# Kernel tuning notes

Hardware: AMD Instinct MI355X
Metric: run time of the kernel (lower is better)

## Reference

```python
import jax, jax.numpy as jnp
import numpy as np

EMBED_DIM = 512
N_HEADS = 8
HEAD_DIM = EMBED_DIM // N_HEADS
SEQ = 4096
BATCH = 2


def setup_inputs() -> dict:
    key = jax.random.key(0)
    k1, k2, k3 = jax.random.split(key, 3)
    x = jax.random.normal(k1, (SEQ, BATCH, EMBED_DIM), dtype=jnp.float32)
    # xavier_uniform for [3E, E]: limit = sqrt(6/(3E+E))
    lim_in = float(np.sqrt(6.0 / (3 * EMBED_DIM + EMBED_DIM)))
    in_proj_weight = jax.random.uniform(k2, (3 * EMBED_DIM, EMBED_DIM), minval=-lim_in, maxval=lim_in, dtype=jnp.float32)
    in_proj_bias = jnp.zeros((3 * EMBED_DIM,), jnp.float32)
    lim_out = float(np.sqrt(1.0 / EMBED_DIM))  # torch Linear default init range
    out_weight = jax.random.uniform(k3, (EMBED_DIM, EMBED_DIM), minval=-lim_out, maxval=lim_out, dtype=jnp.float32)
    out_bias = jnp.zeros((EMBED_DIM,), jnp.float32)
    return {"x": x, "in_proj_weight": in_proj_weight, "in_proj_bias": in_proj_bias,
            "out_weight": out_weight, "out_bias": out_bias}


def reference(x, in_proj_weight, in_proj_bias, out_weight, out_bias):
    # x: [S, B, E] (seq-first, as in the torch module)
    S, B, E = x.shape
    H, D = N_HEADS, HEAD_DIM
    scaling = 1.0 / (D ** 0.5)
    qkv = x @ in_proj_weight.T + in_proj_bias            # [S, B, 3E]
    q, k, v = jnp.split(qkv, 3, axis=-1)                 # each [S, B, E]
    # reshape to [B*H, S, D]
    def to_bh(t):
        return t.reshape(S, B * H, D).transpose(1, 0, 2)
    q = to_bh(q * scaling)
    k = to_bh(k)
    v = to_bh(v)
    scores = jnp.einsum('bqd,bkd->bqk', q, k)            # [B*H, S, S]
    attn = jax.nn.softmax(scores, axis=-1)
    out = jnp.einsum('bqk,bkd->bqd', attn, v)            # [B*H, S, D]
    out = out.transpose(1, 0, 2).reshape(S, B, E)        # [S, B, E]
    return out @ out_weight.T + out_bias
```

## Files before the change

### kernel.cpp

```cpp
#include <hip/hip_runtime.h>

typedef unsigned short u16;
typedef unsigned int   u32;
typedef short bf16x8 __attribute__((ext_vector_type(8)));
typedef float f32x2  __attribute__((ext_vector_type(2)));
typedef float f32x4  __attribute__((ext_vector_type(4)));
typedef float f32x16 __attribute__((ext_vector_type(16)));
typedef u32   u32x4  __attribute__((ext_vector_type(4)));

#define QK_SCALE 0.18033688011112042f

__device__ __forceinline__ u16 f2bf(float f) {
  u32 u = __builtin_bit_cast(u32, f);
  u = (u + 0x7FFFu + ((u >> 16) & 1u)) >> 16;
  return (u16)u;
}

__device__ __forceinline__ u32 cvtpk(float lo, float hi) {
  u32 r;
  asm("v_cvt_pk_bf16_f32 %0, %1, %2" : "=v"(r) : "v"(lo), "v"(hi));
  return r;
}

__device__ __forceinline__ void gload16(void* lds, const void* g) {
  __builtin_amdgcn_global_load_lds(
      (const __attribute__((address_space(1))) u32*)g,
      (__attribute__((address_space(3))) u32*)lds, 16, 0, 0);
}

__device__ __forceinline__ bf16x8 ld8(const void* p) {
  return *(const bf16x8*)p;
}

__global__ __launch_bounds__(256) void cvt_kernel(
    const float* __restrict__ x, const float* __restrict__ w1,
    const float* __restrict__ w2,
    u16* __restrict__ xb, u16* __restrict__ wb, u16* __restrict__ ob) {
  int i = blockIdx.x * 256 + threadIdx.x;
  const float* src; u16* dst; int off;
  if (i < 1048576)            { src = x;  dst = xb; off = i; }
  else if (i < 1048576+196608){ src = w1; dst = wb; off = i - 1048576; }
  else                        { src = w2; dst = ob; off = i - 1245184; }
  float4 v = ((const float4*)src)[off];
  ushort4 o;
  o.x = f2bf(v.x); o.y = f2bf(v.y); o.z = f2bf(v.z); o.w = f2bf(v.w);
  ((ushort4*)dst)[off] = o;
}

template<int MODE>
__global__ __launch_bounds__(256, 2) void gemm_bt(
    const u16* __restrict__ A, const u16* __restrict__ Bm,
    const float* __restrict__ bias,
    u16* __restrict__ q_out, u16* __restrict__ k_out, u16* __restrict__ v_out,
    float* __restrict__ f_out, int M, int N, int K) {
  __shared__ __attribute__((aligned(16))) u16 As[128 * 64];
  __shared__ __attribute__((aligned(16))) u16 Bs[128 * 64];
  const int tid = threadIdx.x, lane = tid & 63, w = tid >> 6;
  const int wm = w >> 1, wn = w & 1;
  const int lo = lane & 15, hi = lane >> 4;
  const int m0 = blockIdx.x * 128, n0 = blockIdx.y * 128;
  f32x4 acc[4][4] = {};
  const int srow = lane >> 3;
  const int skc  = (lane & 7) ^ srow;
  const int nk = K >> 6;
  for (int kt = 0; kt < nk; ++kt) {
    __syncthreads();
    const int k0 = kt * 64;
#pragma unroll
    for (int c = 0; c < 4; ++c) {
      const int ch = w * 4 + c;
      const int row = ch * 8 + srow;
      gload16((char*)As + ch * 1024, A  + (size_t)(m0 + row) * K + k0 + skc * 8);
      gload16((char*)Bs + ch * 1024, Bm + (size_t)(n0 + row) * K + k0 + skc * 8);
    }
    __syncthreads();
#pragma unroll
    for (int kk = 0; kk < 2; ++kk) {
      bf16x8 af[4], bfr[4];
#pragma unroll
      for (int mi = 0; mi < 4; ++mi) {
        const int row = wm * 64 + mi * 16 + lo;
        const int kc = kk * 4 + hi;
        af[mi] = ld8((const char*)As + row * 128 + ((kc ^ (row & 7)) << 4));
      }
#pragma unroll
      for (int ni = 0; ni < 4; ++ni) {
        const int row = wn * 64 + ni * 16 + lo;
        const int kc = kk * 4 + hi;
        bfr[ni] = ld8((const char*)Bs + row * 128 + ((kc ^ (row & 7)) << 4));
      }
#pragma unroll
      for (int mi = 0; mi < 4; ++mi)
#pragma unroll
        for (int ni = 0; ni < 4; ++ni)
          acc[mi][ni] = __builtin_amdgcn_mfma_f32_16x16x32_bf16(
              af[mi], bfr[ni], acc[mi][ni], 0, 0, 0);
    }
  }
#pragma unroll
  for (int mi = 0; mi < 4; ++mi)
#pragma unroll
    for (int ni = 0; ni < 4; ++ni) {
      const int gn = n0 + wn * 64 + ni * 16 + lo;
      const float bv = bias[gn];
#pragma unroll
      for (int r = 0; r < 4; ++r) {
        const int gm = m0 + wm * 64 + mi * 16 + hi * 4 + r;
        float val = acc[mi][ni][r] + bv;
        if (MODE == 0) {
          const int s = gm >> 1, b = gm & 1;
          const int sec = gn >> 9, e = gn & 511;
          const int h = e >> 6, d = e & 63;
          const size_t o = (((size_t)(b * 8 + h) * 4096 + s) << 6) + d;
          if (sec == 0)      q_out[o] = f2bf(val * QK_SCALE);
          else if (sec == 1) k_out[o] = f2bf(val);
          else               v_out[o] = f2bf(val);
        } else {
          f_out[(size_t)gm * N + gn] = val;
        }
      }
    }
}

__global__ __launch_bounds__(256) void transpose_v(
    const u16* __restrict__ v, u16* __restrict__ vt) {
  __shared__ __attribute__((aligned(16))) u16 T[64 * 72];
  const int bh = blockIdx.y, s0 = blockIdx.x * 64;
  const int t = threadIdx.x;
#pragma unroll
  for (int i = 0; i < 2; ++i) {
    const int idx = t + i * 256;
    const int row = idx >> 3, c = idx & 7;
    uint4 d = *(const uint4*)(v + ((size_t)bh * 4096 + s0 + row) * 64 + c * 8);
    *(uint4*)(&T[row * 72 + c * 8]) = d;
  }
  __syncthreads();
#pragma unroll
  for (int i = 0; i < 2; ++i) {
    const int idx = t + i * 256;
    const int dcol = idx >> 3, sc = idx & 7;
    u16 tmp[8];
#pragma unroll
    for (int j = 0; j < 8; ++j) tmp[j] = T[(sc * 8 + j) * 72 + dcol];
    *(uint4*)(vt + ((size_t)bh * 64 + dcol) * 4096 + s0 + sc * 8) = *(const uint4*)tmp;
  }
}

__global__ __launch_bounds__(256, 4) void fa_kernel(
    const u16* __restrict__ q, const u16* __restrict__ k,
    const u16* __restrict__ vt, u16* __restrict__ attn) {
  __shared__ __attribute__((aligned(16))) char S_lds[2][2][8192];
  const int tid = threadIdx.x, lane = tid & 63, w = tid >> 6;
  const int lo = lane & 31, hi5 = lane >> 5;
  const int wq = w & 1;
  const int kvh = w >> 1;
  const int wg = blockIdx.x;
  const int xcd = wg & 7, idx = wg >> 3;
  const int bh = xcd * 2 + (idx >> 6), qb = idx & 63;
  const int q0 = qb * 64 + wq * 32;
  const size_t hb = (size_t)bh * 4096 * 64;
  const u16* kbase = k + hb;
  const u16* vbase = vt + hb;
  bf16x8 qf[4];
#pragma unroll
  for (int ds = 0; ds < 4; ++ds)
    qf[ds] = ld8(q + hb + (size_t)(q0 + lo) * 64 + ds * 16 + hi5 * 8);

  f32x16 acc[2] = {};
  float lrun = 0.f;

  const int srow8 = lane >> 3;
  const int sx    = (lane & 7) ^ srow8;
  const int vda   = (sx >> 2) * 32;
  const int vkc   = sx & 3;
  const int schunk = wq * 2;

#define STAGE(buf, kv0)                                                       \
  {                                                                           \
    char* kb_l = S_lds[kvh][buf];                                             \
    char* vb_l = kb_l + 4096;                                                 \
    _Pragma("unroll")                                                         \
    for (int i = 0; i < 2; ++i) {                                             \
      const int c = schunk + i;                       \
      gload16(kb_l + c * 1024,                                                \
              kbase + (size_t)((kv0) + c * 8 + srow8) * 64 + sx * 8);         \
      gload16(vb_l + c * 1024,                                                \
              vbase + (size_t)(c * 8 + srow8 + vda) * 4096 + (kv0) + vkc * 8);\
    }                                                                         \
  }

  const int kvbase = kvh * 2048;
  STAGE(0, kvbase);
  __syncthreads();

  for (int kb = 0; kb < 64; ++kb) {
    const int cur = kb & 1;
    if (kb < 63) STAGE(cur ^ 1, kvbase + (kb + 1) * 32);
    const char* kl = S_lds[kvh][cur];
    const char* vl = kl + 4096;
    f32x16 st = {};
    __builtin_amdgcn_s_setprio(1);
#pragma unroll
    for (int ds = 0; ds < 4; ++ds) {
      bf16x8 kf = ld8(kl + lo * 128 +
                      ((ds * 32 + hi5 * 16) ^ ((lo & 7) << 4)));
      st = __builtin_amdgcn_mfma_f32_32x32x16_bf16(kf, qf[ds], st, 0, 0, 0);
    }
    __builtin_amdgcn_s_setprio(0);
    float p[16];
    f32x2 lt2; lt2.x = 0.f; lt2.y = 0.f;
#pragma unroll
    for (int i = 0; i < 8; ++i) {
      p[2 * i]     = __builtin_amdgcn_exp2f(st[2 * i]);
      p[2 * i + 1] = __builtin_amdgcn_exp2f(st[2 * i + 1]);
      f32x2 px; px.x = p[2 * i]; px.y = p[2 * i + 1];
      lt2 += px;
    }
    lrun += lt2.x + lt2.y;
#pragma unroll
    for (int ksl = 0; ksl < 2; ++ksl) {
      u32 A0 = cvtpk(p[8 * ksl + 0], p[8 * ksl + 1]);
      u32 A1 = cvtpk(p[8 * ksl + 2], p[8 * ksl + 3]);
      u32 B0 = cvtpk(p[8 * ksl + 4], p[8 * ksl + 5]);
      u32 B1 = cvtpk(p[8 * ksl + 6], p[8 * ksl + 7]);
      asm("v_permlane32_swap_b32 %0, %1" : "+v"(A0), "+v"(B0));
      asm("v_permlane32_swap_b32 %0, %1" : "+v"(A1), "+v"(B1));
      u32x4 pw; pw.x = A0; pw.y = A1; pw.z = B0; pw.w = B1;
      const bf16x8 pa = __builtin_bit_cast(bf16x8, pw);
      __builtin_amdgcn_s_setprio(1);
#pragma unroll
      for (int ds2 = 0; ds2 < 2; ++ds2) {
        bf16x8 vf = ld8(vl + lo * 128 +
                        ((ds2 * 64 + ksl * 32 + hi5 * 16) ^ ((lo & 7) << 4)));
        acc[ds2] = __builtin_amdgcn_mfma_f32_32x32x16_bf16(pa, vf, acc[ds2],
                                                           0, 0, 0);
      }
      __builtin_amdgcn_s_setprio(0);
    }
    __syncthreads();
  }
  lrun += __shfl_xor(lrun, 32);
  float* fl = (float*)S_lds;
  float* Ob = fl;
  float* Ml = fl + 4096;
  if (w >= 2) {
#pragma unroll
    for (int r = 0; r < 16; ++r) {
      const int crow = (r & 3) + 8 * (r >> 2) + 4 * hi5;
#pragma unroll
      for (int ds2 = 0; ds2 < 2; ++ds2)
        Ob[wq * 2048 + crow * 64 + ds2 * 32 + lo] = acc[ds2][r];
    }
    if (hi5 == 0) Ml[wq * 32 + lo] = lrun;
  }
  __syncthreads();
  if (w < 2) {
    const float lB = Ml[wq * 32 + lo];
    const float linv = 1.0f / (lrun + lB);
    const int b = bh >> 3, h = bh & 7;
#pragma unroll
    for (int r = 0; r < 16; ++r) {
      const int crow = (r & 3) + 8 * (r >> 2) + 4 * hi5;
      const float ivR = __shfl(linv, crow);
      const int s = q0 + crow;
#pragma unroll
      for (int ds2 = 0; ds2 < 2; ++ds2) {
        const float ob = Ob[wq * 2048 + crow * 64 + ds2 * 32 + lo];
        attn[(size_t)(s * 2 + b) * 512 + h * 64 + ds2 * 32 + lo] =
            f2bf((acc[ds2][r] + ob) * ivR);
      }
    }
  }
#undef STAGE
}

extern "C" void kernel_launch(void* const* d_in, const int* in_sizes, int n_in,
                              void* d_out, int out_size, void* d_ws, size_t ws_size,
                              hipStream_t stream) {
  const float* x     = (const float*)d_in[0];
  const float* w_in  = (const float*)d_in[1];
  const float* b_in  = (const float*)d_in[2];
  const float* w_out = (const float*)d_in[3];
  const float* b_out = (const float*)d_in[4];
  float* out = (float*)d_out;
  char* ws = (char*)d_ws;
  u16* xb  = (u16*)(ws);
  u16* wb  = (u16*)(ws + 8388608);
  u16* ob  = (u16*)(ws + 9961472);
  u16* qb  = (u16*)(ws + 10485760);
  u16* kb  = (u16*)(ws + 18874368);
  u16* vb  = (u16*)(ws + 27262976);
  u16* vtb = (u16*)(ws + 35651584);
  u16* attn = xb;

  cvt_kernel<<<5120, 256, 0, stream>>>(x, w_in, w_out, xb, wb, ob);
  gemm_bt<0><<<dim3(64, 12), 256, 0, stream>>>(xb, wb, b_in, qb, kb, vb,
                                               nullptr, 8192, 1536, 512);
  transpose_v<<<dim3(64, 16), 256, 0, stream>>>(vb, vtb);
  fa_kernel<<<1024, 256, 0, stream>>>(qb, kb, vtb, attn);
  gemm_bt<1><<<dim3(64, 4), 256, 0, stream>>>(attn, ob, b_out, nullptr, nullptr,
                                              nullptr, out, 8192, 512, 512);
}
```

Measured before the change: 142.2 us.

## Process two 32-row query tiles per wave to reuse K/V fragments

Each wave now handles 64 query rows, as two 32-row tiles A and B, instead of 32, so every K and V fragment loaded from LDS feeds two MFMAs. The grid is halved to 512 blocks, launch bounds drop to 2 waves per SIMD to make room for the doubled registers, and the row-sum buffer moves to its own shared array because the cross-wave merge buffer now fills S_lds. This cuts LDS reads and K/V staging per query row. The cost is higher register pressure, lower occupancy and fewer blocks, which may leave CUs underfilled.

```diff
diff --git a/kernel.cpp b/kernel.cpp
--- a/kernel.cpp
+++ b/kernel.cpp
@@ -146,28 +146,31 @@
   }
 }
 
-__global__ __launch_bounds__(256, 4) void fa_kernel(
+__global__ __launch_bounds__(256, 2) void fa_kernel(
     const u16* __restrict__ q, const u16* __restrict__ k,
     const u16* __restrict__ vt, u16* __restrict__ attn) {
   __shared__ __attribute__((aligned(16))) char S_lds[2][2][8192];
+  __shared__ float Ml[2][2][32];
   const int tid = threadIdx.x, lane = tid & 63, w = tid >> 6;
   const int lo = lane & 31, hi5 = lane >> 5;
   const int wq = w & 1;
   const int kvh = w >> 1;
   const int wg = blockIdx.x;
   const int xcd = wg & 7, idx = wg >> 3;
-  const int bh = xcd * 2 + (idx >> 6), qb = idx & 63;
-  const int q0 = qb * 64 + wq * 32;
+  const int bh = xcd * 2 + (idx >> 5), qb = idx & 31;
+  const int q0 = qb * 128 + wq * 64;
   const size_t hb = (size_t)bh * 4096 * 64;
   const u16* kbase = k + hb;
   const u16* vbase = vt + hb;
-  bf16x8 qf[4];
-#pragma unroll
-  for (int ds = 0; ds < 4; ++ds)
-    qf[ds] = ld8(q + hb + (size_t)(q0 + lo) * 64 + ds * 16 + hi5 * 8);
-
-  f32x16 acc[2] = {};
-  float lrun = 0.f;
+  bf16x8 qfA[4], qfB[4];
+#pragma unroll
+  for (int ds = 0; ds < 4; ++ds) {
+    qfA[ds] = ld8(q + hb + (size_t)(q0 + lo) * 64 + ds * 16 + hi5 * 8);
+    qfB[ds] = ld8(q + hb + (size_t)(q0 + 32 + lo) * 64 + ds * 16 + hi5 * 8);
+  }
+
+  f32x16 accA[2] = {}, accB[2] = {};
+  float lrunA = 0.f, lrunB = 0.f;
 
   const int srow8 = lane >> 3;
   const int sx    = (lane & 7) ^ srow8;
@@ -189,6 +192,18 @@
     }                                                                         \
   }
 
+#define PACK(stv, ksl, pa)                                                    \
+  {                                                                           \
+    u32 A0 = cvtpk(stv[8 * ksl + 0], stv[8 * ksl + 1]);                       \
+    u32 A1 = cvtpk(stv[8 * ksl + 2], stv[8 * ksl + 3]);                       \
+    u32 B0 = cvtpk(stv[8 * ksl + 4], stv[8 * ksl + 5]);                       \
+    u32 B1 = cvtpk(stv[8 * ksl + 6], stv[8 * ksl + 7]);                       \
+    asm("v_permlane32_swap_b32 %0, %1" : "+v"(A0), "+v"(B0));                 \
+    asm("v_permlane32_swap_b32 %0, %1" : "+v"(A1), "+v"(B1));                 \
+    u32x4 pw; pw.x = A0; pw.y = A1; pw.z = B0; pw.w = B1;                     \
+    pa = __builtin_bit_cast(bf16x8, pw);                                      \
+  }
+
   const int kvbase = kvh * 2048;
   STAGE(0, kvbase);
   __syncthreads();
@@ -198,80 +213,89 @@
     if (kb < 63) STAGE(cur ^ 1, kvbase + (kb + 1) * 32);
     const char* kl = S_lds[kvh][cur];
     const char* vl = kl + 4096;
-    f32x16 st = {};
+    f32x16 stA = {}, stB = {};
     __builtin_amdgcn_s_setprio(1);
 #pragma unroll
     for (int ds = 0; ds < 4; ++ds) {
       bf16x8 kf = ld8(kl + lo * 128 +
                       ((ds * 32 + hi5 * 16) ^ ((lo & 7) << 4)));
-      st = __builtin_amdgcn_mfma_f32_32x32x16_bf16(kf, qf[ds], st, 0, 0, 0);
+      stA = __builtin_amdgcn_mfma_f32_32x32x16_bf16(kf, qfA[ds], stA, 0, 0, 0);
+      stB = __builtin_amdgcn_mfma_f32_32x32x16_bf16(kf, qfB[ds], stB, 0, 0, 0);
     }
     __builtin_amdgcn_s_setprio(0);
-    float p[16];
-    f32x2 lt2; lt2.x = 0.f; lt2.y = 0.f;
+    f32x2 ltA; ltA.x = 0.f; ltA.y = 0.f;
+    f32x2 ltB; ltB.x = 0.f; ltB.y = 0.f;
 #pragma unroll
     for (int i = 0; i < 8; ++i) {
-      p[2 * i]     = __builtin_amdgcn_exp2f(st[2 * i]);
-      p[2 * i + 1] = __builtin_amdgcn_exp2f(st[2 * i + 1]);
-      f32x2 px; px.x = p[2 * i]; px.y = p[2 * i + 1];
-      lt2 += px;
-    }
-    lrun += lt2.x + lt2.y;
+      stA[2 * i]     = __builtin_amdgcn_exp2f(stA[2 * i]);
+      stA[2 * i + 1] = __builtin_amdgcn_exp2f(stA[2 * i + 1]);
+      f32x2 pa2; pa2.x = stA[2 * i]; pa2.y = stA[2 * i + 1];
+      ltA += pa2;
+      stB[2 * i]     = __builtin_amdgcn_exp2f(stB[2 * i]);
+      stB[2 * i + 1] = __builtin_amdgcn_exp2f(stB[2 * i + 1]);
+      f32x2 pb2; pb2.x = stB[2 * i]; pb2.y = stB[2 * i + 1];
+      ltB += pb2;
+    }
+    lrunA += ltA.x + ltA.y;
+    lrunB += ltB.x + ltB.y;
 #pragma unroll
     for (int ksl = 0; ksl < 2; ++ksl) {
-      u32 A0 = cvtpk(p[8 * ksl + 0], p[8 * ksl + 1]);
-      u32 A1 = cvtpk(p[8 * ksl + 2], p[8 * ksl + 3]);
-      u32 B0 = cvtpk(p[8 * ksl + 4], p[8 * ksl + 5]);
-      u32 B1 = cvtpk(p[8 * ksl + 6], p[8 * ksl + 7]);
-      asm("v_permlane32_swap_b32 %0, %1" : "+v"(A0), "+v"(B0));
-      asm("v_permlane32_swap_b32 %0, %1" : "+v"(A1), "+v"(B1));
-      u32x4 pw; pw.x = A0; pw.y = A1; pw.z = B0; pw.w = B1;
-      const bf16x8 pa = __builtin_bit_cast(bf16x8, pw);
+      bf16x8 paA, paB;
+      PACK(stA, ksl, paA);
+      PACK(stB, ksl, paB);
       __builtin_amdgcn_s_setprio(1);
 #pragma unroll
       for (int ds2 = 0; ds2 < 2; ++ds2) {
         bf16x8 vf = ld8(vl + lo * 128 +
                         ((ds2 * 64 + ksl * 32 + hi5 * 16) ^ ((lo & 7) << 4)));
-        acc[ds2] = __builtin_amdgcn_mfma_f32_32x32x16_bf16(pa, vf, acc[ds2],
-                                                           0, 0, 0);
+        accA[ds2] = __builtin_amdgcn_mfma_f32_32x32x16_bf16(paA, vf, accA[ds2],
+                                                            0, 0, 0);
+        accB[ds2] = __builtin_amdgcn_mfma_f32_32x32x16_bf16(paB, vf, accB[ds2],
+                                                            0, 0, 0);
       }
       __builtin_amdgcn_s_setprio(0);
     }
     __syncthreads();
   }
-  lrun += __shfl_xor(lrun, 32);
-  float* fl = (float*)S_lds;
-  float* Ob = fl;
-  float* Ml = fl + 4096;
+  lrunA += __shfl_xor(lrunA, 32);
+  lrunB += __shfl_xor(lrunB, 32);
+  float* Ob = (float*)S_lds;
   if (w >= 2) {
 #pragma unroll
     for (int r = 0; r < 16; ++r) {
       const int crow = (r & 3) + 8 * (r >> 2) + 4 * hi5;
 #pragma unroll
-      for (int ds2 = 0; ds2 < 2; ++ds2)
-        Ob[wq * 2048 + crow * 64 + ds2 * 32 + lo] = acc[ds2][r];
-    }
-    if (hi5 == 0) Ml[wq * 32 + lo] = lrun;
+      for (int ds2 = 0; ds2 < 2; ++ds2) {
+        Ob[((wq * 2 + 0) * 32 + crow) * 64 + ds2 * 32 + lo] = accA[ds2][r];
+        Ob[((wq * 2 + 1) * 32 + crow) * 64 + ds2 * 32 + lo] = accB[ds2][r];
+      }
+    }
+    if (hi5 == 0) { Ml[wq][0][lo] = lrunA; Ml[wq][1][lo] = lrunB; }
   }
   __syncthreads();
   if (w < 2) {
-    const float lB = Ml[wq * 32 + lo];
-    const float linv = 1.0f / (lrun + lB);
+    const float linvA = 1.0f / (lrunA + Ml[wq][0][lo]);
+    const float linvB = 1.0f / (lrunB + Ml[wq][1][lo]);
     const int b = bh >> 3, h = bh & 7;
 #pragma unroll
     for (int r = 0; r < 16; ++r) {
       const int crow = (r & 3) + 8 * (r >> 2) + 4 * hi5;
-      const float ivR = __shfl(linv, crow);
-      const int s = q0 + crow;
+      const float ivA = __shfl(linvA, crow);
+      const float ivB = __shfl(linvB, crow);
+      const int sA = q0 + crow, sB = q0 + 32 + crow;
 #pragma unroll
       for (int ds2 = 0; ds2 < 2; ++ds2) {
-        const float ob = Ob[wq * 2048 + crow * 64 + ds2 * 32 + lo];
-        attn[(size_t)(s * 2 + b) * 512 + h * 64 + ds2 * 32 + lo] =
-            f2bf((acc[ds2][r] + ob) * ivR);
+        const float oA = Ob[((wq * 2 + 0) * 32 + crow) * 64 + ds2 * 32 + lo];
+        const float oB = Ob[((wq * 2 + 1) * 32 + crow) * 64 + ds2 * 32 + lo];
+        attn[(size_t)(sA * 2 + b) * 512 + h * 64 + ds2 * 32 + lo] =
+            f2bf((accA[ds2][r] + oA) * ivA);
+        attn[(size_t)(sB * 2 + b) * 512 + h * 64 + ds2 * 32 + lo] =
+            f2bf((accB[ds2][r] + oB) * ivB);
       }
     }
   }
 #undef STAGE
+#undef PACK
 }
 
 extern "C" void kernel_launch(void* const* d_in, const int* in_sizes, int n_in,
@@ -297,7 +321,7 @@
   gemm_bt<0><<<dim3(64, 12), 256, 0, stream>>>(xb, wb, b_in, qb, kb, vb,
                                                nullptr, 8192, 1536, 512);
   transpose_v<<<dim3(64, 16), 256, 0, stream>>>(vb, vtb);
-  fa_kernel<<<1024, 256, 0, stream>>>(qb, kb, vtb, attn);
+  fa_kernel<<<512, 256, 0, stream>>>(qb, kb, vtb, attn);
   gemm_bt<1><<<dim3(64, 4), 256, 0, stream>>>(attn, ob, b_out, nullptr, nullptr,
                                               nullptr, out, 8192, 512, 512);
 }
```

After: 138.7 us. -2.5%, faster.

## Stage only K in LDS with 64-key tiles, load V fragments directly from global

Applied to the files above, without the earlier changes.

The flash-attention inner loop now processes 64 keys per iteration instead of 32, staging only K tiles through double-buffered LDS. V fragments are read straight from global memory into registers rather than going through LDS. This halves the number of loop iterations and barriers and frees LDS capacity. The cost is uncoalesced, latency-exposed global loads for V inside the loop and higher register pressure from the eight V fragments and two score tiles.

```diff
diff --git a/kernel.cpp b/kernel.cpp
--- a/kernel.cpp
+++ b/kernel.cpp
@@ -149,7 +149,8 @@
 __global__ __launch_bounds__(256, 4) void fa_kernel(
     const u16* __restrict__ q, const u16* __restrict__ k,
     const u16* __restrict__ vt, u16* __restrict__ attn) {
-  __shared__ __attribute__((aligned(16))) char S_lds[2][2][8192];
+  __shared__ __attribute__((aligned(16))) char K_lds[2][2][8192];
+  __shared__ float Ml[2][32];
   const int tid = threadIdx.x, lane = tid & 63, w = tid >> 6;
   const int lo = lane & 31, hi5 = lane >> 5;
   const int wq = w & 1;
@@ -171,92 +172,105 @@
 
   const int srow8 = lane >> 3;
   const int sx    = (lane & 7) ^ srow8;
-  const int vda   = (sx >> 2) * 32;
-  const int vkc   = sx & 3;
-  const int schunk = wq * 2;
+  const int schunk = wq * 4;
 
 #define STAGE(buf, kv0)                                                       \
   {                                                                           \
-    char* kb_l = S_lds[kvh][buf];                                             \
-    char* vb_l = kb_l + 4096;                                                 \
+    char* kb_l = K_lds[kvh][buf];                                             \
     _Pragma("unroll")                                                         \
-    for (int i = 0; i < 2; ++i) {                                             \
+    for (int i = 0; i < 4; ++i) {                                             \
       const int c = schunk + i;                       \
       gload16(kb_l + c * 1024,                                                \
               kbase + (size_t)((kv0) + c * 8 + srow8) * 64 + sx * 8);         \
-      gload16(vb_l + c * 1024,                                                \
-              vbase + (size_t)(c * 8 + srow8 + vda) * 4096 + (kv0) + vkc * 8);\
     }                                                                         \
+  }
+
+#define PACK(stv, ksl, pa)                                                    \
+  {                                                                           \
+    u32 A0 = cvtpk(stv[8 * ksl + 0], stv[8 * ksl + 1]);                       \
+    u32 A1 = cvtpk(stv[8 * ksl + 2], stv[8 * ksl + 3]);                       \
+    u32 B0 = cvtpk(stv[8 * ksl + 4], stv[8 * ksl + 5]);                       \
+    u32 B1 = cvtpk(stv[8 * ksl + 6], stv[8 * ksl + 7]);                       \
+    asm("v_permlane32_swap_b32 %0, %1" : "+v"(A0), "+v"(B0));                 \
+    asm("v_permlane32_swap_b32 %0, %1" : "+v"(A1), "+v"(B1));                 \
+    u32x4 pw; pw.x = A0; pw.y = A1; pw.z = B0; pw.w = B1;                     \
+    pa = __builtin_bit_cast(bf16x8, pw);                                      \
   }
 
   const int kvbase = kvh * 2048;
   STAGE(0, kvbase);
   __syncthreads();
 
-  for (int kb = 0; kb < 64; ++kb) {
-    const int cur = kb & 1;
-    if (kb < 63) STAGE(cur ^ 1, kvbase + (kb + 1) * 32);
-    const char* kl = S_lds[kvh][cur];
-    const char* vl = kl + 4096;
-    f32x16 st = {};
+  for (int t = 0; t < 32; ++t) {
+    const int cur = t & 1;
+    const int kv0 = kvbase + t * 64;
+    if (t < 31) STAGE(cur ^ 1, kv0 + 64);
+    const char* kl = K_lds[kvh][cur];
+    f32x16 st0 = {}, st1 = {};
     __builtin_amdgcn_s_setprio(1);
 #pragma unroll
     for (int ds = 0; ds < 4; ++ds) {
-      bf16x8 kf = ld8(kl + lo * 128 +
-                      ((ds * 32 + hi5 * 16) ^ ((lo & 7) << 4)));
-      st = __builtin_amdgcn_mfma_f32_32x32x16_bf16(kf, qf[ds], st, 0, 0, 0);
+      const int r0 = lo, r1 = 32 + lo;
+      const int col = ds * 32 + hi5 * 16;
+      bf16x8 kf0 = ld8(kl + r0 * 128 + (col ^ ((r0 & 7) << 4)));
+      bf16x8 kf1 = ld8(kl + r1 * 128 + (col ^ ((r1 & 7) << 4)));
+      st0 = __builtin_amdgcn_mfma_f32_32x32x16_bf16(kf0, qf[ds], st0, 0, 0, 0);
+      st1 = __builtin_amdgcn_mfma_f32_32x32x16_bf16(kf1, qf[ds], st1, 0, 0, 0);
     }
     __builtin_amdgcn_s_setprio(0);
-    float p[16];
-    f32x2 lt2; lt2.x = 0.f; lt2.y = 0.f;
+    bf16x8 vf[8];
+#pragma unroll
+    for (int sl = 0; sl < 4; ++sl)
+#pragma unroll
+      for (int ds2 = 0; ds2 < 2; ++ds2)
+        vf[sl * 2 + ds2] = ld8(vbase + (size_t)(ds2 * 32 + lo) * 4096 +
+                               kv0 + sl * 16 + hi5 * 8);
+    f32x2 lt; lt.x = 0.f; lt.y = 0.f;
 #pragma unroll
     for (int i = 0; i < 8; ++i) {
-      p[2 * i]     = __builtin_amdgcn_exp2f(st[2 * i]);
-      p[2 * i + 1] = __builtin_amdgcn_exp2f(st[2 * i + 1]);
-      f32x2 px; px.x = p[2 * i]; px.y = p[2 * i + 1];
-      lt2 += px;
-    }
-    lrun += lt2.x + lt2.y;
-#pragma unroll
-    for (int ksl = 0; ksl < 2; ++ksl) {
-      u32 A0 = cvtpk(p[8 * ksl + 0], p[8 * ksl + 1]);
-      u32 A1 = cvtpk(p[8 * ksl + 2], p[8 * ksl + 3]);
-      u32 B0 = cvtpk(p[8 * ksl + 4], p[8 * ksl + 5]);
-      u32 B1 = cvtpk(p[8 * ksl + 6], p[8 * ksl + 7]);
-      asm("v_permlane32_swap_b32 %0, %1" : "+v"(A0), "+v"(B0));
-      asm("v_permlane32_swap_b32 %0, %1" : "+v"(A1), "+v"(B1));
-      u32x4 pw; pw.x = A0; pw.y = A1; pw.z = B0; pw.w = B1;
-      const bf16x8 pa = __builtin_bit_cast(bf16x8, pw);
-      __builtin_amdgcn_s_setprio(1);
-#pragma unroll
-      for (int ds2 = 0; ds2 < 2; ++ds2) {
-        bf16x8 vf = ld8(vl + lo * 128 +
-                        ((ds2 * 64 + ksl * 32 + hi5 * 16) ^ ((lo & 7) << 4)));
-        acc[ds2] = __builtin_amdgcn_mfma_f32_32x32x16_bf16(pa, vf, acc[ds2],
-                                                           0, 0, 0);
-      }
-      __builtin_amdgcn_s_setprio(0);
-    }
+      st0[2*i]   = __builtin_amdgcn_exp2f(st0[2*i]);
+      st0[2*i+1] = __builtin_amdgcn_exp2f(st0[2*i+1]);
+      f32x2 e0; e0.x = st0[2*i]; e0.y = st0[2*i+1]; lt += e0;
+      st1[2*i]   = __builtin_amdgcn_exp2f(st1[2*i]);
+      st1[2*i+1] = __builtin_amdgcn_exp2f(st1[2*i+1]);
+      f32x2 e1; e1.x = st1[2*i]; e1.y = st1[2*i+1]; lt += e1;
+    }
+    lrun += lt.x + lt.y;
+    bf16x8 pa0, pa1, pa2, pa3;
+    PACK(st0, 0, pa0); PACK(st0, 1, pa1);
+    PACK(st1, 0, pa2); PACK(st1, 1, pa3);
+    __builtin_amdgcn_s_setprio(1);
+#pragma unroll
+    for (int ds2 = 0; ds2 < 2; ++ds2) {
+      acc[ds2] = __builtin_amdgcn_mfma_f32_32x32x16_bf16(pa0, vf[0 + ds2],
+                                                         acc[ds2], 0, 0, 0);
+      acc[ds2] = __builtin_amdgcn_mfma_f32_32x32x16_bf16(pa1, vf[2 + ds2],
+                                                         acc[ds2], 0, 0, 0);
+      acc[ds2] = __builtin_amdgcn_mfma_f32_32x32x16_bf16(pa2, vf[4 + ds2],
+                                                         acc[ds2], 0, 0, 0);
+      acc[ds2] = __builtin_amdgcn_mfma_f32_32x32x16_bf16(pa3, vf[6 + ds2],
+                                                         acc[ds2], 0, 0, 0);
+    }
+    __builtin_amdgcn_s_setprio(0);
     __syncthreads();
   }
+
   lrun += __shfl_xor(lrun, 32);
-  float* fl = (float*)S_lds;
-  float* Ob = fl;
-  float* Ml = fl + 4096;
+  __syncthreads();
+  float* Ob = (float*)K_lds;
   if (w >= 2) {
 #pragma unroll
     for (int r = 0; r < 16; ++r) {
       const int crow = (r & 3) + 8 * (r >> 2) + 4 * hi5;
 #pragma unroll
       for (int ds2 = 0; ds2 < 2; ++ds2)
-        Ob[wq * 2048 + crow * 64 + ds2 * 32 + lo] = acc[ds2][r];
-    }
-    if (hi5 == 0) Ml[wq * 32 + lo] = lrun;
+        Ob[(wq * 32 + crow) * 64 + ds2 * 32 + lo] = acc[ds2][r];
+    }
+    if (hi5 == 0) Ml[wq][lo] = lrun;
   }
   __syncthreads();
   if (w < 2) {
-    const float lB = Ml[wq * 32 + lo];
-    const float linv = 1.0f / (lrun + lB);
+    const float linv = 1.0f / (lrun + Ml[wq][lo]);
     const int b = bh >> 3, h = bh & 7;
 #pragma unroll
     for (int r = 0; r < 16; ++r) {
@@ -265,13 +279,14 @@
       const int s = q0 + crow;
 #pragma unroll
       for (int ds2 = 0; ds2 < 2; ++ds2) {
-        const float ob = Ob[wq * 2048 + crow * 64 + ds2 * 32 + lo];
+        const float ob = Ob[(wq * 32 + crow) * 64 + ds2 * 32 + lo];
         attn[(size_t)(s * 2 + b) * 512 + h * 64 + ds2 * 32 + lo] =
             f2bf((acc[ds2][r] + ob) * ivR);
       }
     }
   }
 #undef STAGE
+#undef PACK
 }
 
 extern "C" void kernel_launch(void* const* d_in, const int* in_sizes, int n_in,
```

Result: slower. 237.7 us (+67.2%).
